# Kernel optimization log

Hardware: AMD Instinct MI355X
Metric: run time of the kernel (lower is better)

Reference implementation:

```python
import jax, jax.numpy as jnp
import numpy as np

N_NODES = 50000
N_EDGES = 1600000
NFEAT, NHID, NCLASS = 512, 256, 64


def _mpnn_layer(x, src, dst, W, b, num_nodes):
    # linear transform then mean aggregation over incoming edges (incl. self loops)
    h = x @ W + b                      # [N, out]
    msg = h[src]                       # gather along edges [E+N, out]
    agg = jax.ops.segment_sum(msg, dst, num_segments=num_nodes)
    ones = jnp.ones((src.shape[0],), dtype=x.dtype)
    cnt = jax.ops.segment_sum(ones, dst, num_segments=num_nodes)
    return agg / jnp.maximum(cnt, 1.0)[:, None]


def setup_inputs() -> dict:
    key = jax.random.key(0)
    k1, k2, k3, k4, k5, k6 = jax.random.split(key, 6)
    x = jax.random.normal(k1, (N_NODES, NFEAT), dtype=jnp.float32)
    edge_index = jax.random.randint(k2, (2, N_EDGES), 0, N_NODES, dtype=jnp.int64)
    W1 = jax.random.normal(k3, (NFEAT, NHID), dtype=jnp.float32) * (1.0 / np.sqrt(NFEAT))
    b1 = jax.random.normal(k4, (NHID,), dtype=jnp.float32) * 0.01
    W2 = jax.random.normal(k5, (NHID, NCLASS), dtype=jnp.float32) * (1.0 / np.sqrt(NHID))
    b2 = jax.random.normal(k6, (NCLASS,), dtype=jnp.float32) * 0.01
    return {"x": x, "edge_index": edge_index, "W1": W1, "b1": b1, "W2": W2, "b2": b2}


def reference(x, edge_index, W1, b1, W2, b2):
    n = x.shape[0]
    # add self loops (done once per layer in the original; edge set identical)
    loops = jnp.arange(n, dtype=edge_index.dtype)
    src = jnp.concatenate([edge_index[0], loops])
    dst = jnp.concatenate([edge_index[1], loops])

    h = _mpnn_layer(x, src, dst, W1, b1, n)
    h = jax.nn.relu(h)
    # dropout is identity at inference
    h = _mpnn_layer(h, src, dst, W2, b2, n)
    return jax.nn.log_softmax(h, axis=1)
```

## Files before the change

kernel.cpp:

```cpp
#include <hip/hip_runtime.h>
#include <math.h>

#define NN 50000
#define NE 1600000
#define NF 512
#define NH 256
#define NC 64
#define CAP 96
#define NBKT 98
#define BCAP 18432
#define G1_BLOCKS 391
#define P1_BLOCKS 196

typedef short bf16x8 __attribute__((ext_vector_type(8)));
typedef float f32x4  __attribute__((ext_vector_type(4)));
typedef float f32x2  __attribute__((ext_vector_type(2)));

__device__ __forceinline__ float bf2f(unsigned short u) {
    return __uint_as_float(((unsigned)u) << 16);
}
__device__ __forceinline__ unsigned short f2bf(float f) {
    unsigned u = __float_as_uint(f);
    unsigned r = (u + 0x7FFF + ((u >> 16) & 1)) >> 16;
    return (unsigned short)r;
}

__device__ __forceinline__ unsigned char f2e4m3(float f) {
#if __has_builtin(__builtin_amdgcn_cvt_pk_fp8_f32)
    int v = __builtin_amdgcn_cvt_pk_fp8_f32(f, f, 0, false);
    return (unsigned char)(v & 0xff);
#else
    unsigned u = __float_as_uint(f);
    unsigned s = (u >> 31) << 7;
    float a = fabsf(f);
    if (a >= 448.f) return (unsigned char)(s | 0x7E);
    int e32 = (int)((u >> 23) & 0xff) - 127;
    if (e32 < -6) {
        int m = (int)rintf(a * 512.f);
        return (unsigned char)(s | m);
    }
    unsigned mant = u & 0x7fffff;
    unsigned keep = mant >> 20;
    unsigned rest = mant & 0xfffff;
    if (rest > 0x80000 || (rest == 0x80000 && (keep & 1))) keep++;
    int e8 = e32 + 7;
    if (keep == 8) { keep = 0; e8++; }
    if (e8 >= 16 || (e8 == 15 && keep == 7)) return (unsigned char)(s | 0x7E);
    return (unsigned char)(s | (e8 << 3) | keep);
#endif
}

__device__ __forceinline__ void dec4(unsigned int u, float& x0, float& x1, float& x2, float& x3) {
#if __has_builtin(__builtin_amdgcn_cvt_pk_f32_fp8)
    f32x2 lo = __builtin_amdgcn_cvt_pk_f32_fp8(u, false);
    f32x2 hi = __builtin_amdgcn_cvt_pk_f32_fp8(u, true);
    x0 = lo[0]; x1 = lo[1]; x2 = hi[0]; x3 = hi[1];
#else
    float r[4];
    #pragma unroll
    for (int i = 0; i < 4; ++i) {
        unsigned b = (u >> (8 * i)) & 0xff;
        unsigned s = (b >> 7) & 1, e = (b >> 3) & 15, m = b & 7;
        float v = e ? __uint_as_float(((e + 120u) << 23) | (m << 20))
                    : (float)m * 0.001953125f;
        r[i] = s ? -v : v;
    }
    x0 = r[0]; x1 = r[1]; x2 = r[2]; x3 = r[3];
#endif
}

__global__ __launch_bounds__(256)
void prep(const float* __restrict__ W1, const float* __restrict__ W2,
          unsigned short* __restrict__ w1t, unsigned short* __restrict__ w2t,
          const int* __restrict__ ei, int2* __restrict__ pairs, int* __restrict__ cursor) {
    __shared__ int bcnt[NBKT];
    __shared__ int bpos[NBKT];
    const int b = blockIdx.x;
    const int t = threadIdx.x;
    if (b < NF) {
        w1t[(size_t)t * NF + b] = f2bf(W1[(size_t)b * NH + t]);
        return;
    }
    if (b < NF + NH) {
        const int k = b - NF;
        if (t < NC) w2t[(size_t)t * NH + k] = f2bf(W2[(size_t)k * NC + t]);
        return;
    }
    const int fb = b - NF - NH;
    const int base = fb * 8192;
    for (int i = t; i < NBKT; i += 256) bcnt[i] = 0;
    __syncthreads();
    int ds[32], ss[32];
    #pragma unroll
    for (int k = 0; k < 32; ++k) {
        const int e = base + k * 256 + t;
        if (e < NE) {
            ds[k] = ei[NE + e];
            ss[k] = ei[e];
            atomicAdd(&bcnt[ds[k] >> 9], 1);
        } else ds[k] = -1;
    }
    __syncthreads();
    for (int i = t; i < NBKT; i += 256) bpos[i] = atomicAdd(&cursor[i], bcnt[i]);
    __syncthreads();
    #pragma unroll
    for (int k = 0; k < 32; ++k) {
        if (ds[k] >= 0) {
            const int bkt = ds[k] >> 9;
            const int p = atomicAdd(&bcnt[bkt], -1) - 1;
            const int g = bpos[bkt] + p;
            if (g < BCAP) {
                int2 v; v.x = ds[k]; v.y = ss[k];
                pairs[(size_t)bkt * BCAP + g] = v;
            }
        }
    }
}

__global__ __launch_bounds__(512)
void gemm1_fill(const float* __restrict__ A, const unsigned short* __restrict__ BT,
                const float* __restrict__ bias, unsigned char* __restrict__ C,
                const int2* __restrict__ pairs, const int* __restrict__ cursor,
                int* __restrict__ deg, int* __restrict__ csr) {
    __shared__ unsigned short As[128][40];
    __shared__ unsigned short Bs[256][40];
    __shared__ int ldeg[512];
    const int tid = threadIdx.x;

    if (blockIdx.x >= G1_BLOCKS) {
        const int fb = blockIdx.x - G1_BLOCKS;
        const int nb = fb * 512;
        ldeg[tid] = 0;
        __syncthreads();
        int cnt = cursor[fb];
        if (cnt > BCAP) cnt = BCAP;
        const int2* pb = pairs + (size_t)fb * BCAP;
        for (int i = tid; i < cnt; i += 512) {
            const int2 e = pb[i];
            const int p = atomicAdd(&ldeg[e.x & 511], 1);
            if (p < CAP) csr[(size_t)e.x * CAP + p] = e.y;
        }
        __syncthreads();
        const int node = nb + tid;
        if (node < NN) deg[node] = ldeg[tid];
        return;
    }

    const int w    = tid >> 6, lane = tid & 63;
    const int wr   = w >> 2,   wc   = w & 3;
    const int bm   = blockIdx.x * 128;
    const int rl   = lane & 15;
    const int ko   = (lane >> 4) * 8;

    f32x4 acc[4][4] = {};

    for (int k0 = 0; k0 < NF; k0 += 32) {
        {
            const int row = tid >> 2;
            const int kc  = (tid & 3) * 8;
            const int gr  = bm + row;
            float4 v0 = make_float4(0.f, 0.f, 0.f, 0.f), v1 = v0;
            if (gr < NN) {
                const float4* p = reinterpret_cast<const float4*>(A + (size_t)gr * NF + k0 + kc);
                v0 = p[0]; v1 = p[1];
            }
            bf16x8 pk;
            pk[0] = (short)f2bf(v0.x); pk[1] = (short)f2bf(v0.y);
            pk[2] = (short)f2bf(v0.z); pk[3] = (short)f2bf(v0.w);
            pk[4] = (short)f2bf(v1.x); pk[5] = (short)f2bf(v1.y);
            pk[6] = (short)f2bf(v1.z); pk[7] = (short)f2bf(v1.w);
            *reinterpret_cast<bf16x8*>(&As[row][kc]) = pk;
        }
        {
            const int row = tid >> 1;
            const int kc  = (tid & 1) * 16;
            const bf16x8* p = reinterpret_cast<const bf16x8*>(BT + (size_t)row * NF + k0 + kc);
            *reinterpret_cast<bf16x8*>(&Bs[row][kc])     = p[0];
            *reinterpret_cast<bf16x8*>(&Bs[row][kc + 8]) = p[1];
        }
        __syncthreads();

        bf16x8 af[4], bfr[4];
        #pragma unroll
        for (int m = 0; m < 4; ++m)
            af[m] = *reinterpret_cast<const bf16x8*>(&As[wr * 64 + m * 16 + rl][ko]);
        #pragma unroll
        for (int n = 0; n < 4; ++n)
            bfr[n] = *reinterpret_cast<const bf16x8*>(&Bs[wc * 64 + n * 16 + rl][ko]);
        #pragma unroll
        for (int m = 0; m < 4; ++m)
            #pragma unroll
            for (int n = 0; n < 4; ++n)
                acc[m][n] = __builtin_amdgcn_mfma_f32_16x16x32_bf16(af[m], bfr[n], acc[m][n], 0, 0, 0);
        __syncthreads();
    }

    float bv[4];
    #pragma unroll
    for (int n = 0; n < 4; ++n) bv[n] = bias[wc * 64 + n * 16 + rl];
    #pragma unroll
    for (int m = 0; m < 4; ++m) {
        #pragma unroll
        for (int j = 0; j < 4; ++j) {
            const int row = bm + wr * 64 + m * 16 + (lane >> 4) * 4 + j;
            if (row < NN) {
                #pragma unroll
                for (int n = 0; n < 4; ++n) {
                    const int col = wc * 64 + n * 16 + rl;
                    C[(size_t)row * NH + col] = f2e4m3(acc[m][n][j] + bv[n]);
                }
            }
        }
    }
}

__global__ __launch_bounds__(256)
void gemm2_mfma(const unsigned short* __restrict__ A, const unsigned short* __restrict__ BT,
                const float* __restrict__ bias, unsigned short* __restrict__ C) {
    __shared__ unsigned short As[128][40];
    __shared__ unsigned short Bs[64][40];
    const int tid = threadIdx.x;
    const int w = tid >> 6, lane = tid & 63;
    const int bm = blockIdx.x * 128;
    const int rl = lane & 15, ko = (lane >> 4) * 8;

    f32x4 acc[2][4] = {};

    for (int k0 = 0; k0 < NH; k0 += 32) {
        #pragma unroll
        for (int h = 0; h < 2; ++h) {
            const int c = tid + h * 256;
            const int row = c >> 2, kc = (c & 3) * 8;
            const int gr = bm + row;
            bf16x8 v = {};
            if (gr < NN) v = *reinterpret_cast<const bf16x8*>(A + (size_t)gr * NH + k0 + kc);
            *reinterpret_cast<bf16x8*>(&As[row][kc]) = v;
        }
        {
            const int row = tid >> 2, kc = (tid & 3) * 8;
            *reinterpret_cast<bf16x8*>(&Bs[row][kc]) =
                *reinterpret_cast<const bf16x8*>(BT + (size_t)row * NH + k0 + kc);
        }
        __syncthreads();

        bf16x8 af[2], bfr[4];
        #pragma unroll
        for (int m = 0; m < 2; ++m)
            af[m] = *reinterpret_cast<const bf16x8*>(&As[w * 32 + m * 16 + rl][ko]);
        #pragma unroll
        for (int n = 0; n < 4; ++n)
            bfr[n] = *reinterpret_cast<const bf16x8*>(&Bs[n * 16 + rl][ko]);
        #pragma unroll
        for (int m = 0; m < 2; ++m)
            #pragma unroll
            for (int n = 0; n < 4; ++n)
                acc[m][n] = __builtin_amdgcn_mfma_f32_16x16x32_bf16(af[m], bfr[n], acc[m][n], 0, 0, 0);
        __syncthreads();
    }

    float bv[4];
    #pragma unroll
    for (int n = 0; n < 4; ++n) bv[n] = bias[n * 16 + rl];
    #pragma unroll
    for (int m = 0; m < 2; ++m) {
        #pragma unroll
        for (int j = 0; j < 4; ++j) {
            const int row = bm + w * 32 + m * 16 + (lane >> 4) * 4 + j;
            if (row < NN) {
                #pragma unroll
                for (int n = 0; n < 4; ++n)
                    C[(size_t)row * NC + n * 16 + rl] = f2bf(acc[m][n][j] + bv[n]);
            }
        }
    }
}

__global__ __launch_bounds__(256)
void agg_relu(const unsigned char* __restrict__ hf, const int* __restrict__ deg,
              const int* __restrict__ csr, unsigned short* __restrict__ o) {
    const int node = blockIdx.x * 4 + (threadIdx.x >> 6);
    const int lane = threadIdx.x & 63;
    if (node >= NN) return;
    const int dcnt = min(deg[node], CAP);
    const int beg = node * CAP, end = beg + dcnt;
    const unsigned int* hfu = reinterpret_cast<const unsigned int*>(hf);
    const size_t loff = lane;

    float a0, a1, a2, a3;
    dec4(hfu[(size_t)node * 64 + loff], a0, a1, a2, a3);

    #define LD1(EE) hfu[(size_t)csr[EE] * 64 + loff]
    #define ACC1(U) { float b0,b1,b2,b3; dec4(U,b0,b1,b2,b3); a0+=b0; a1+=b1; a2+=b2; a3+=b3; }

    int e = beg;
    if (end - e >= 8) {
        unsigned u0 = LD1(e+0), u1 = LD1(e+1), u2 = LD1(e+2), u3 = LD1(e+3);
        unsigned u4 = LD1(e+4), u5 = LD1(e+5), u6 = LD1(e+6), u7 = LD1(e+7);
        e += 8;
        for (; e + 8 <= end; e += 8) {
            const unsigned v0 = LD1(e+0), v1 = LD1(e+1), v2 = LD1(e+2), v3 = LD1(e+3);
            const unsigned v4 = LD1(e+4), v5 = LD1(e+5), v6 = LD1(e+6), v7 = LD1(e+7);
            ACC1(u0) ACC1(u1) ACC1(u2) ACC1(u3)
            ACC1(u4) ACC1(u5) ACC1(u6) ACC1(u7)
            u0 = v0; u1 = v1; u2 = v2; u3 = v3;
            u4 = v4; u5 = v5; u6 = v6; u7 = v7;
        }
        ACC1(u0) ACC1(u1) ACC1(u2) ACC1(u3)
        ACC1(u4) ACC1(u5) ACC1(u6) ACC1(u7)
    }
    for (; e < end; ++e) { const unsigned u = LD1(e); ACC1(u) }
    #undef LD1
    #undef ACC1

    const float inv = 1.0f / (float)(dcnt + 1);
    ushort4 r;
    r.x = f2bf(fmaxf(a0 * inv, 0.f));
    r.y = f2bf(fmaxf(a1 * inv, 0.f));
    r.z = f2bf(fmaxf(a2 * inv, 0.f));
    r.w = f2bf(fmaxf(a3 * inv, 0.f));
    *reinterpret_cast<ushort4*>(o + (size_t)node * NH + lane * 4) = r;
}

__global__ __launch_bounds__(256)
void agg2_softmax(const unsigned short* __restrict__ h2, const int* __restrict__ deg,
                  const int* __restrict__ csr, float* __restrict__ out) {
    const int node = blockIdx.x * 8 + (threadIdx.x >> 5);
    const int l = threadIdx.x & 31;
    if (node >= NN) return;
    const int dcnt = min(deg[node], CAP);
    const int beg = node * CAP, end = beg + dcnt;
    const unsigned int* h2u = reinterpret_cast<const unsigned int*>(h2);

    unsigned int su = h2u[(size_t)node * 32 + l];
    float a0 = bf2f((unsigned short)(su & 0xffff));
    float a1 = bf2f((unsigned short)(su >> 16));

    #define LD2(EE) h2u[(size_t)csr[EE] * 32 + l]
    #define ACC2(U) { a0 += bf2f((unsigned short)((U) & 0xffff)); a1 += bf2f((unsigned short)((U) >> 16)); }

    int e = beg;
    if (end - e >= 8) {
        unsigned u0 = LD2(e+0), u1 = LD2(e+1), u2 = LD2(e+2), u3 = LD2(e+3);
        unsigned u4 = LD2(e+4), u5 = LD2(e+5), u6 = LD2(e+6), u7 = LD2(e+7);
        e += 8;
        for (; e + 8 <= end; e += 8) {
            const unsigned v0 = LD2(e+0), v1 = LD2(e+1), v2 = LD2(e+2), v3 = LD2(e+3);
            const unsigned v4 = LD2(e+4), v5 = LD2(e+5), v6 = LD2(e+6), v7 = LD2(e+7);
            ACC2(u0) ACC2(u1) ACC2(u2) ACC2(u3)
            ACC2(u4) ACC2(u5) ACC2(u6) ACC2(u7)
            u0 = v0; u1 = v1; u2 = v2; u3 = v3;
            u4 = v4; u5 = v5; u6 = v6; u7 = v7;
        }
        ACC2(u0) ACC2(u1) ACC2(u2) ACC2(u3)
        ACC2(u4) ACC2(u5) ACC2(u6) ACC2(u7)
    }
    for (; e < end; ++e) { const unsigned u = LD2(e); ACC2(u) }
    #undef LD2
    #undef ACC2

    const float inv = 1.0f / (float)(dcnt + 1);
    a0 *= inv; a1 *= inv;

    float m = fmaxf(a0, a1);
    #pragma unroll
    for (int o = 16; o > 0; o >>= 1) m = fmaxf(m, __shfl_xor(m, o));
    float s = expf(a0 - m) + expf(a1 - m);
    #pragma unroll
    for (int o = 16; o > 0; o >>= 1) s += __shfl_xor(s, o);
    const float lg = logf(s);
    float2 r;
    r.x = a0 - m - lg;
    r.y = a1 - m - lg;
    *reinterpret_cast<float2*>(out + (size_t)node * NC + l * 2) = r;
}

extern "C" void kernel_launch(void* const* d_in, const int* in_sizes, int n_in,
                              void* d_out, int out_size, void* d_ws, size_t ws_size,
                              hipStream_t stream) {
    const float* x  = (const float*)d_in[0];
    const int*   ei = (const int*)d_in[1];
    const float* W1 = (const float*)d_in[2];
    const float* b1 = (const float*)d_in[3];
    const float* W2 = (const float*)d_in[4];
    const float* b2 = (const float*)d_in[5];
    float* out = (float*)d_out;

    char* ws = (char*)d_ws;
    unsigned short* hr     = (unsigned short*)(ws);
    unsigned char*  h1f    = (unsigned char*)(ws + 25600000);
    unsigned short* h2b    = (unsigned short*)(ws + 38400000);
    unsigned short* w1t    = (unsigned short*)(ws + 44800000);
    unsigned short* w2t    = (unsigned short*)(ws + 45062144);
    int*            deg    = (int*)(ws + 45094912);
    int*            csr    = (int*)(ws + 45294912);
    int2*           pairs  = (int2*)(ws + 64494912);
    int*            cursor = (int*)(ws + 78945600);

    hipMemsetAsync(cursor, 0, NBKT * sizeof(int), stream);

    prep<<<NF + NH + P1_BLOCKS, 256, 0, stream>>>(W1, W2, w1t, w2t, ei, pairs, cursor);

    gemm1_fill<<<G1_BLOCKS + NBKT, 512, 0, stream>>>(x, w1t, b1, h1f, pairs, cursor, deg, csr);

    agg_relu<<<(NN + 3) / 4, 256, 0, stream>>>(h1f, deg, csr, hr);

    gemm2_mfma<<<(NN + 127) / 128, 256, 0, stream>>>(hr, w2t, b2, h2b);

    agg2_softmax<<<(NN + 7) / 8, 256, 0, stream>>>(h2b, deg, csr, out);
}
```

Baseline: 166.0 us.

## Fuse layer-1 aggregation with layer-2 GEMM and pad CSR rows to sixteen

Merges the layer-1 mean aggregation and ReLU with the second GEMM. Each block aggregates 64 nodes into shared memory and multiplies them by W2 with MFMA, so the bf16 hidden matrix no longer makes a round trip through global memory and one launch goes away. CSR rows are padded to a multiple of 16 with a sentinel node whose feature rows are zeroed, which lets the gather loops run unrolled by 16 without a scalar tail. GEMM1 moves to 64-row tiles with 256 threads, doubling the block count. The cost is extra wasted gathers on padded entries, and the fused kernel reads W2 straight from global memory.

```diff
diff --git a/kernel.cpp b/kernel.cpp
--- a/kernel.cpp
+++ b/kernel.cpp
@@ -9,7 +9,7 @@
 #define CAP 96
 #define NBKT 98
 #define BCAP 18432
-#define G1_BLOCKS 391
+#define G1B 782
 #define P1_BLOCKS 196
 
 typedef short bf16x8 __attribute__((ext_vector_type(8)));
@@ -72,7 +72,8 @@
 __global__ __launch_bounds__(256)
 void prep(const float* __restrict__ W1, const float* __restrict__ W2,
           unsigned short* __restrict__ w1t, unsigned short* __restrict__ w2t,
-          const int* __restrict__ ei, int2* __restrict__ pairs, int* __restrict__ cursor) {
+          const int* __restrict__ ei, int2* __restrict__ pairs, int* __restrict__ cursor,
+          unsigned char* __restrict__ h1f, unsigned short* __restrict__ h2b) {
     __shared__ int bcnt[NBKT];
     __shared__ int bpos[NBKT];
     const int b = blockIdx.x;
@@ -84,6 +85,11 @@
     if (b < NF + NH) {
         const int k = b - NF;
         if (t < NC) w2t[(size_t)t * NH + k] = f2bf(W2[(size_t)k * NC + t]);
+        return;
+    }
+    if (b == NF + NH + P1_BLOCKS) {
+        if (t < 64) reinterpret_cast<unsigned int*>(h1f)[(size_t)NN * 64 + t] = 0u;
+        if (t < 32) reinterpret_cast<unsigned int*>(h2b)[(size_t)NN * 32 + t] = 0u;
         return;
     }
     const int fb = b - NF - NH;
@@ -117,38 +123,47 @@
     }
 }
 
-__global__ __launch_bounds__(512)
+__global__ __launch_bounds__(256)
 void gemm1_fill(const float* __restrict__ A, const unsigned short* __restrict__ BT,
                 const float* __restrict__ bias, unsigned char* __restrict__ C,
                 const int2* __restrict__ pairs, const int* __restrict__ cursor,
                 int* __restrict__ deg, int* __restrict__ csr) {
-    __shared__ unsigned short As[128][40];
+    __shared__ unsigned short As[64][40];
     __shared__ unsigned short Bs[256][40];
     __shared__ int ldeg[512];
     const int tid = threadIdx.x;
 
-    if (blockIdx.x >= G1_BLOCKS) {
-        const int fb = blockIdx.x - G1_BLOCKS;
+    if (blockIdx.x >= G1B) {
+        const int fb = blockIdx.x - G1B;
         const int nb = fb * 512;
-        ldeg[tid] = 0;
+        ldeg[tid] = 0; ldeg[tid + 256] = 0;
         __syncthreads();
         int cnt = cursor[fb];
         if (cnt > BCAP) cnt = BCAP;
         const int2* pb = pairs + (size_t)fb * BCAP;
-        for (int i = tid; i < cnt; i += 512) {
+        for (int i = tid; i < cnt; i += 256) {
             const int2 e = pb[i];
             const int p = atomicAdd(&ldeg[e.x & 511], 1);
             if (p < CAP) csr[(size_t)e.x * CAP + p] = e.y;
         }
         __syncthreads();
-        const int node = nb + tid;
-        if (node < NN) deg[node] = ldeg[tid];
+        #pragma unroll
+        for (int h = 0; h < 2; ++h) {
+            const int ln = tid + h * 256;
+            const int node = nb + ln;
+            if (node < NN) {
+                const int d = ldeg[ln];
+                deg[node] = d;
+                const int dc = min(d, CAP);
+                const int pd = min((dc + 15) & ~15, CAP);
+                for (int p = dc; p < pd; ++p) csr[(size_t)node * CAP + p] = NN;
+            }
+        }
         return;
     }
 
     const int w    = tid >> 6, lane = tid & 63;
-    const int wr   = w >> 2,   wc   = w & 3;
-    const int bm   = blockIdx.x * 128;
+    const int bm   = blockIdx.x * 64;
     const int rl   = lane & 15;
     const int ko   = (lane >> 4) * 8;
 
@@ -172,21 +187,21 @@
             *reinterpret_cast<bf16x8*>(&As[row][kc]) = pk;
         }
         {
-            const int row = tid >> 1;
-            const int kc  = (tid & 1) * 16;
-            const bf16x8* p = reinterpret_cast<const bf16x8*>(BT + (size_t)row * NF + k0 + kc);
-            *reinterpret_cast<bf16x8*>(&Bs[row][kc])     = p[0];
-            *reinterpret_cast<bf16x8*>(&Bs[row][kc + 8]) = p[1];
+            const bf16x8* p = reinterpret_cast<const bf16x8*>(BT + (size_t)tid * NF + k0);
+            *reinterpret_cast<bf16x8*>(&Bs[tid][0])  = p[0];
+            *reinterpret_cast<bf16x8*>(&Bs[tid][8])  = p[1];
+            *reinterpret_cast<bf16x8*>(&Bs[tid][16]) = p[2];
+            *reinterpret_cast<bf16x8*>(&Bs[tid][24]) = p[3];
         }
         __syncthreads();
 
         bf16x8 af[4], bfr[4];
         #pragma unroll
         for (int m = 0; m < 4; ++m)
-            af[m] = *reinterpret_cast<const bf16x8*>(&As[wr * 64 + m * 16 + rl][ko]);
+            af[m] = *reinterpret_cast<const bf16x8*>(&As[m * 16 + rl][ko]);
         #pragma unroll
         for (int n = 0; n < 4; ++n)
-            bfr[n] = *reinterpret_cast<const bf16x8*>(&Bs[wc * 64 + n * 16 + rl][ko]);
+            bfr[n] = *reinterpret_cast<const bf16x8*>(&Bs[w * 64 + n * 16 + rl][ko]);
         #pragma unroll
         for (int m = 0; m < 4; ++m)
             #pragma unroll
@@ -197,16 +212,16 @@
 
     float bv[4];
     #pragma unroll
-    for (int n = 0; n < 4; ++n) bv[n] = bias[wc * 64 + n * 16 + rl];
+    for (int n = 0; n < 4; ++n) bv[n] = bias[w * 64 + n * 16 + rl];
     #pragma unroll
     for (int m = 0; m < 4; ++m) {
         #pragma unroll
         for (int j = 0; j < 4; ++j) {
-            const int row = bm + wr * 64 + m * 16 + (lane >> 4) * 4 + j;
+            const int row = bm + m * 16 + (lane >> 4) * 4 + j;
             if (row < NN) {
                 #pragma unroll
                 for (int n = 0; n < 4; ++n) {
-                    const int col = wc * 64 + n * 16 + rl;
+                    const int col = w * 64 + n * 16 + rl;
                     C[(size_t)row * NH + col] = f2e4m3(acc[m][n][j] + bv[n]);
                 }
             }
@@ -214,111 +229,95 @@
     }
 }
 
-__global__ __launch_bounds__(256)
-void gemm2_mfma(const unsigned short* __restrict__ A, const unsigned short* __restrict__ BT,
-                const float* __restrict__ bias, unsigned short* __restrict__ C) {
-    __shared__ unsigned short As[128][40];
-    __shared__ unsigned short Bs[64][40];
+__global__ __launch_bounds__(512)
+void agg_gemm2(const unsigned char* __restrict__ hf, const int* __restrict__ deg,
+               const int* __restrict__ csr, const unsigned short* __restrict__ w2t,
+               const float* __restrict__ b2, unsigned short* __restrict__ h2b) {
+    __shared__ unsigned short hrs[64][264];
     const int tid = threadIdx.x;
     const int w = tid >> 6, lane = tid & 63;
-    const int bm = blockIdx.x * 128;
-    const int rl = lane & 15, ko = (lane >> 4) * 8;
-
-    f32x4 acc[2][4] = {};
-
-    for (int k0 = 0; k0 < NH; k0 += 32) {
-        #pragma unroll
-        for (int h = 0; h < 2; ++h) {
-            const int c = tid + h * 256;
-            const int row = c >> 2, kc = (c & 3) * 8;
-            const int gr = bm + row;
-            bf16x8 v = {};
-            if (gr < NN) v = *reinterpret_cast<const bf16x8*>(A + (size_t)gr * NH + k0 + kc);
-            *reinterpret_cast<bf16x8*>(&As[row][kc]) = v;
-        }
-        {
-            const int row = tid >> 2, kc = (tid & 3) * 8;
-            *reinterpret_cast<bf16x8*>(&Bs[row][kc]) =
-                *reinterpret_cast<const bf16x8*>(BT + (size_t)row * NH + k0 + kc);
-        }
-        __syncthreads();
-
-        bf16x8 af[2], bfr[4];
-        #pragma unroll
-        for (int m = 0; m < 2; ++m)
-            af[m] = *reinterpret_cast<const bf16x8*>(&As[w * 32 + m * 16 + rl][ko]);
-        #pragma unroll
-        for (int n = 0; n < 4; ++n)
-            bfr[n] = *reinterpret_cast<const bf16x8*>(&Bs[n * 16 + rl][ko]);
-        #pragma unroll
-        for (int m = 0; m < 2; ++m)
-            #pragma unroll
-            for (int n = 0; n < 4; ++n)
-                acc[m][n] = __builtin_amdgcn_mfma_f32_16x16x32_bf16(af[m], bfr[n], acc[m][n], 0, 0, 0);
-        __syncthreads();
-    }
-
-    float bv[4];
-    #pragma unroll
-    for (int n = 0; n < 4; ++n) bv[n] = bias[n * 16 + rl];
-    #pragma unroll
-    for (int m = 0; m < 2; ++m) {
-        #pragma unroll
-        for (int j = 0; j < 4; ++j) {
-            const int row = bm + w * 32 + m * 16 + (lane >> 4) * 4 + j;
-            if (row < NN) {
-                #pragma unroll
-                for (int n = 0; n < 4; ++n)
-                    C[(size_t)row * NC + n * 16 + rl] = f2bf(acc[m][n][j] + bv[n]);
-            }
-        }
-    }
-}
-
-__global__ __launch_bounds__(256)
-void agg_relu(const unsigned char* __restrict__ hf, const int* __restrict__ deg,
-              const int* __restrict__ csr, unsigned short* __restrict__ o) {
-    const int node = blockIdx.x * 4 + (threadIdx.x >> 6);
-    const int lane = threadIdx.x & 63;
-    if (node >= NN) return;
-    const int dcnt = min(deg[node], CAP);
-    const int beg = node * CAP, end = beg + dcnt;
+    const int nb = blockIdx.x * 64;
     const unsigned int* hfu = reinterpret_cast<const unsigned int*>(hf);
     const size_t loff = lane;
 
-    float a0, a1, a2, a3;
-    dec4(hfu[(size_t)node * 64 + loff], a0, a1, a2, a3);
-
-    #define LD1(EE) hfu[(size_t)csr[EE] * 64 + loff]
-    #define ACC1(U) { float b0,b1,b2,b3; dec4(U,b0,b1,b2,b3); a0+=b0; a1+=b1; a2+=b2; a3+=b3; }
-
-    int e = beg;
-    if (end - e >= 8) {
-        unsigned u0 = LD1(e+0), u1 = LD1(e+1), u2 = LD1(e+2), u3 = LD1(e+3);
-        unsigned u4 = LD1(e+4), u5 = LD1(e+5), u6 = LD1(e+6), u7 = LD1(e+7);
-        e += 8;
-        for (; e + 8 <= end; e += 8) {
-            const unsigned v0 = LD1(e+0), v1 = LD1(e+1), v2 = LD1(e+2), v3 = LD1(e+3);
-            const unsigned v4 = LD1(e+4), v5 = LD1(e+5), v6 = LD1(e+6), v7 = LD1(e+7);
-            ACC1(u0) ACC1(u1) ACC1(u2) ACC1(u3)
-            ACC1(u4) ACC1(u5) ACC1(u6) ACC1(u7)
-            u0 = v0; u1 = v1; u2 = v2; u3 = v3;
-            u4 = v4; u5 = v5; u6 = v6; u7 = v7;
-        }
-        ACC1(u0) ACC1(u1) ACC1(u2) ACC1(u3)
-        ACC1(u4) ACC1(u5) ACC1(u6) ACC1(u7)
-    }
-    for (; e < end; ++e) { const unsigned u = LD1(e); ACC1(u) }
-    #undef LD1
-    #undef ACC1
-
-    const float inv = 1.0f / (float)(dcnt + 1);
-    ushort4 r;
-    r.x = f2bf(fmaxf(a0 * inv, 0.f));
-    r.y = f2bf(fmaxf(a1 * inv, 0.f));
-    r.z = f2bf(fmaxf(a2 * inv, 0.f));
-    r.w = f2bf(fmaxf(a3 * inv, 0.f));
-    *reinterpret_cast<ushort4*>(o + (size_t)node * NH + lane * 4) = r;
+    #define LDA(EE) hfu[(size_t)csr[EE] * 64 + loff]
+    #define ACCA(U) { float b0,b1,b2_,b3; dec4(U,b0,b1,b2_,b3); a0+=b0; a1+=b1; a2+=b2_; a3+=b3; }
+    for (int r = 0; r < 8; ++r) {
+        const int ln = w * 8 + r;
+        const int node = nb + ln;
+        if (node < NN) {
+            const int dcnt = min(deg[node], CAP);
+            const int pad = (dcnt + 15) & ~15;
+            float a0, a1, a2, a3;
+            dec4(hfu[(size_t)node * 64 + loff], a0, a1, a2, a3);
+            int e = node * CAP;
+            const int eend = e + pad;
+            if (pad > 0) {
+                unsigned u0=LDA(e+0),u1=LDA(e+1),u2=LDA(e+2),u3=LDA(e+3),
+                         u4=LDA(e+4),u5=LDA(e+5),u6=LDA(e+6),u7=LDA(e+7),
+                         u8=LDA(e+8),u9=LDA(e+9),u10=LDA(e+10),u11=LDA(e+11),
+                         u12=LDA(e+12),u13=LDA(e+13),u14=LDA(e+14),u15=LDA(e+15);
+                e += 16;
+                for (; e < eend; e += 16) {
+                    unsigned t;
+                    t=LDA(e+0);  ACCA(u0)  u0=t;
+                    t=LDA(e+1);  ACCA(u1)  u1=t;
+                    t=LDA(e+2);  ACCA(u2)  u2=t;
+                    t=LDA(e+3);  ACCA(u3)  u3=t;
+                    t=LDA(e+4);  ACCA(u4)  u4=t;
+                    t=LDA(e+5);  ACCA(u5)  u5=t;
+                    t=LDA(e+6);  ACCA(u6)  u6=t;
+                    t=LDA(e+7);  ACCA(u7)  u7=t;
+                    t=LDA(e+8);  ACCA(u8)  u8=t;
+                    t=LDA(e+9);  ACCA(u9)  u9=t;
+                    t=LDA(e+10); ACCA(u10) u10=t;
+                    t=LDA(e+11); ACCA(u11) u11=t;
+                    t=LDA(e+12); ACCA(u12) u12=t;
+                    t=LDA(e+13); ACCA(u13) u13=t;
+                    t=LDA(e+14); ACCA(u14) u14=t;
+                    t=LDA(e+15); ACCA(u15) u15=t;
+                }
+                ACCA(u0) ACCA(u1) ACCA(u2) ACCA(u3) ACCA(u4) ACCA(u5) ACCA(u6) ACCA(u7)
+                ACCA(u8) ACCA(u9) ACCA(u10) ACCA(u11) ACCA(u12) ACCA(u13) ACCA(u14) ACCA(u15)
+            }
+            const float inv = 1.0f / (float)(dcnt + 1);
+            ushort4 rr;
+            rr.x = f2bf(fmaxf(a0 * inv, 0.f));
+            rr.y = f2bf(fmaxf(a1 * inv, 0.f));
+            rr.z = f2bf(fmaxf(a2 * inv, 0.f));
+            rr.w = f2bf(fmaxf(a3 * inv, 0.f));
+            *reinterpret_cast<ushort4*>(&hrs[ln][lane * 4]) = rr;
+        } else {
+            ushort4 z; z.x = z.y = z.z = z.w = 0;
+            *reinterpret_cast<ushort4*>(&hrs[ln][lane * 4]) = z;
+        }
+    }
+    #undef LDA
+    #undef ACCA
+    __syncthreads();
+
+    const int mw = w >> 1, nh = w & 1;
+    const int rl = lane & 15, ko = (lane >> 4) * 8;
+    f32x4 acc2[2] = {};
+    for (int k0 = 0; k0 < NH; k0 += 32) {
+        const bf16x8 af = *reinterpret_cast<const bf16x8*>(&hrs[mw * 16 + rl][k0 + ko]);
+        #pragma unroll
+        for (int j = 0; j < 2; ++j) {
+            const int c = (nh * 2 + j) * 16 + rl;
+            const bf16x8 bf = *reinterpret_cast<const bf16x8*>(w2t + (size_t)c * NH + k0 + ko);
+            acc2[j] = __builtin_amdgcn_mfma_f32_16x16x32_bf16(af, bf, acc2[j], 0, 0, 0);
+        }
+    }
+    const float bv0 = b2[(nh * 2 + 0) * 16 + rl];
+    const float bv1 = b2[(nh * 2 + 1) * 16 + rl];
+    #pragma unroll
+    for (int j2 = 0; j2 < 4; ++j2) {
+        const int row = nb + mw * 16 + (lane >> 4) * 4 + j2;
+        if (row < NN) {
+            h2b[(size_t)row * NC + (nh * 2 + 0) * 16 + rl] = f2bf(acc2[0][j2] + bv0);
+            h2b[(size_t)row * NC + (nh * 2 + 1) * 16 + rl] = f2bf(acc2[1][j2] + bv1);
+        }
+    }
 }
 
 __global__ __launch_bounds__(256)
@@ -328,35 +327,47 @@
     const int l = threadIdx.x & 31;
     if (node >= NN) return;
     const int dcnt = min(deg[node], CAP);
-    const int beg = node * CAP, end = beg + dcnt;
+    const int pad = (dcnt + 15) & ~15;
     const unsigned int* h2u = reinterpret_cast<const unsigned int*>(h2);
 
     unsigned int su = h2u[(size_t)node * 32 + l];
     float a0 = bf2f((unsigned short)(su & 0xffff));
     float a1 = bf2f((unsigned short)(su >> 16));
 
-    #define LD2(EE) h2u[(size_t)csr[EE] * 32 + l]
-    #define ACC2(U) { a0 += bf2f((unsigned short)((U) & 0xffff)); a1 += bf2f((unsigned short)((U) >> 16)); }
-
-    int e = beg;
-    if (end - e >= 8) {
-        unsigned u0 = LD2(e+0), u1 = LD2(e+1), u2 = LD2(e+2), u3 = LD2(e+3);
-        unsigned u4 = LD2(e+4), u5 = LD2(e+5), u6 = LD2(e+6), u7 = LD2(e+7);
-        e += 8;
-        for (; e + 8 <= end; e += 8) {
-            const unsigned v0 = LD2(e+0), v1 = LD2(e+1), v2 = LD2(e+2), v3 = LD2(e+3);
-            const unsigned v4 = LD2(e+4), v5 = LD2(e+5), v6 = LD2(e+6), v7 = LD2(e+7);
-            ACC2(u0) ACC2(u1) ACC2(u2) ACC2(u3)
-            ACC2(u4) ACC2(u5) ACC2(u6) ACC2(u7)
-            u0 = v0; u1 = v1; u2 = v2; u3 = v3;
-            u4 = v4; u5 = v5; u6 = v6; u7 = v7;
-        }
-        ACC2(u0) ACC2(u1) ACC2(u2) ACC2(u3)
-        ACC2(u4) ACC2(u5) ACC2(u6) ACC2(u7)
-    }
-    for (; e < end; ++e) { const unsigned u = LD2(e); ACC2(u) }
-    #undef LD2
-    #undef ACC2
+    #define LDB(EE) h2u[(size_t)csr[EE] * 32 + l]
+    #define ACCB(U) { a0 += bf2f((unsigned short)((U) & 0xffff)); a1 += bf2f((unsigned short)((U) >> 16)); }
+    int e = node * CAP;
+    const int eend = e + pad;
+    if (pad > 0) {
+        unsigned u0=LDB(e+0),u1=LDB(e+1),u2=LDB(e+2),u3=LDB(e+3),
+                 u4=LDB(e+4),u5=LDB(e+5),u6=LDB(e+6),u7=LDB(e+7),
+                 u8=LDB(e+8),u9=LDB(e+9),u10=LDB(e+10),u11=LDB(e+11),
+                 u12=LDB(e+12),u13=LDB(e+13),u14=LDB(e+14),u15=LDB(e+15);
+        e += 16;
+        for (; e < eend; e += 16) {
+            unsigned t;
+            t=LDB(e+0);  ACCB(u0)  u0=t;
+            t=LDB(e+1);  ACCB(u1)  u1=t;
+            t=LDB(e+2);  ACCB(u2)  u2=t;
+            t=LDB(e+3);  ACCB(u3)  u3=t;
+            t=LDB(e+4);  ACCB(u4)  u4=t;
+            t=LDB(e+5);  ACCB(u5)  u5=t;
+            t=LDB(e+6);  ACCB(u6)  u6=t;
+            t=LDB(e+7);  ACCB(u7)  u7=t;
+            t=LDB(e+8);  ACCB(u8)  u8=t;
+            t=LDB(e+9);  ACCB(u9)  u9=t;
+            t=LDB(e+10); ACCB(u10) u10=t;
+            t=LDB(e+11); ACCB(u11) u11=t;
+            t=LDB(e+12); ACCB(u12) u12=t;
+            t=LDB(e+13); ACCB(u13) u13=t;
+            t=LDB(e+14); ACCB(u14) u14=t;
+            t=LDB(e+15); ACCB(u15) u15=t;
+        }
+        ACCB(u0) ACCB(u1) ACCB(u2) ACCB(u3) ACCB(u4) ACCB(u5) ACCB(u6) ACCB(u7)
+        ACCB(u8) ACCB(u9) ACCB(u10) ACCB(u11) ACCB(u12) ACCB(u13) ACCB(u14) ACCB(u15)
+    }
+    #undef LDB
+    #undef ACCB
 
     const float inv = 1.0f / (float)(dcnt + 1);
     a0 *= inv; a1 *= inv;
@@ -386,25 +397,22 @@
     float* out = (float*)d_out;
 
     char* ws = (char*)d_ws;
-    unsigned short* hr     = (unsigned short*)(ws);
-    unsigned char*  h1f    = (unsigned char*)(ws + 25600000);
-    unsigned short* h2b    = (unsigned short*)(ws + 38400000);
-    unsigned short* w1t    = (unsigned short*)(ws + 44800000);
-    unsigned short* w2t    = (unsigned short*)(ws + 45062144);
-    int*            deg    = (int*)(ws + 45094912);
-    int*            csr    = (int*)(ws + 45294912);
-    int2*           pairs  = (int2*)(ws + 64494912);
-    int*            cursor = (int*)(ws + 78945600);
+    unsigned char*  h1f    = (unsigned char*)(ws);
+    unsigned short* h2b    = (unsigned short*)(ws + 12800512);
+    unsigned short* w1t    = (unsigned short*)(ws + 19200768);
+    unsigned short* w2t    = (unsigned short*)(ws + 19462912);
+    int*            deg    = (int*)(ws + 19495680);
+    int*            csr    = (int*)(ws + 19695680);
+    int2*           pairs  = (int2*)(ws + 38895680);
+    int*            cursor = (int*)(ws + 53346368);
 
     hipMemsetAsync(cursor, 0, NBKT * sizeof(int), stream);
 
-    prep<<<NF + NH + P1_BLOCKS, 256, 0, stream>>>(W1, W2, w1t, w2t, ei, pairs, cursor);
-
-    gemm1_fill<<<G1_BLOCKS + NBKT, 512, 0, stream>>>(x, w1t, b1, h1f, pairs, cursor, deg, csr);
-
-    agg_relu<<<(NN + 3) / 4, 256, 0, stream>>>(h1f, deg, csr, hr);
-
-    gemm2_mfma<<<(NN + 127) / 128, 256, 0, stream>>>(hr, w2t, b2, h2b);
+    prep<<<NF + NH + P1_BLOCKS + 1, 256, 0, stream>>>(W1, W2, w1t, w2t, ei, pairs, cursor, h1f, h2b);
+
+    gemm1_fill<<<G1B + NBKT, 256, 0, stream>>>(x, w1t, b1, h1f, pairs, cursor, deg, csr);
+
+    agg_gemm2<<<(NN + 63) / 64, 512, 0, stream>>>(h1f, deg, csr, w2t, b2, h2b);
 
     agg2_softmax<<<(NN + 7) / 8, 256, 0, stream>>>(h2b, deg, csr, out);
 }
```

Measured after the change: 195.5 us. 17.8% more time.
